# Performance work log

Measured on AMD Instinct MI355X. Metric: run time of the kernel, lower is better.

The kernel has to match this reference:

```python
import jax, jax.numpy as jnp
import numpy as np

USER_NUM = 100000
ITEM_NUM = 50000
N_NODES = USER_NUM + ITEM_NUM
HIDE_DIM = 64
N_EDGES = 4000000
LAYER_NUM = 3


def setup_inputs() -> dict:
    key = jax.random.key(0)
    k1, k2, k3, k4 = jax.random.split(key, 4)
    # Xavier uniform for embeddings: bound = sqrt(6/(fan_in+fan_out))
    bound_u = float(np.sqrt(6.0 / (USER_NUM + HIDE_DIM)))
    bound_i = float(np.sqrt(6.0 / (ITEM_NUM + HIDE_DIM)))
    user_emb = jax.random.uniform(k1, (USER_NUM, HIDE_DIM), jnp.float32, -bound_u, bound_u)
    item_emb = jax.random.uniform(k2, (ITEM_NUM, HIDE_DIM), jnp.float32, -bound_i, bound_i)
    src = jax.random.randint(k3, (N_EDGES,), 0, N_NODES, dtype=jnp.int32)
    dst = jax.random.randint(k4, (N_EDGES,), 0, N_NODES, dtype=jnp.int32)
    return {"user_emb": user_emb, "item_emb": item_emb, "src": src, "dst": dst}


def _gcn_layer(node_f, src, dst, out_norm, in_norm):
    # node_f: [N, D]; symmetric degree-normalized SpMM (copy_u + sum)
    h = node_f * out_norm  # pre-scale by out_degree^-0.5
    agg = jax.ops.segment_sum(h[src], dst, num_segments=N_NODES)
    return agg * in_norm  # post-scale by in_degree^-0.5


def reference(user_emb, item_emb, src, dst):
    ones = jnp.ones((N_EDGES,), jnp.float32)
    out_deg = jnp.clip(jax.ops.segment_sum(ones, src, num_segments=N_NODES), 1.0)
    in_deg = jnp.clip(jax.ops.segment_sum(ones, dst, num_segments=N_NODES), 1.0)
    out_norm = (out_deg ** -0.5)[:, None]
    in_norm = (in_deg ** -0.5)[:, None]

    res_user = user_emb
    res_item = item_emb
    for i in range(LAYER_NUM):
        if i == 0:
            node_f = jnp.concatenate([res_user, res_item], axis=0)
        else:
            node_f = embeddings
        embeddings = _gcn_layer(node_f, src, dst, out_norm, in_norm)
        scale = 1.0 / (i + 2)
        res_user = res_user + embeddings[:USER_NUM] * scale
        res_item = res_item + embeddings[USER_NUM:] * scale
    return (res_user, res_item)
```

## Files before the change

kernel.cpp:

```cpp
#include <hip/hip_runtime.h>
#include <stdint.h>

#define USER_NUM 100000
#define ITEM_NUM 50000
#define N_NODES  150000
#define HIDE_DIM 64
#define N_EDGES  4000000
#define SLAB     72

#define HRANGES 3
#define RNODES  50000
#define RWORDS  (RNODES / 4)
#define SLICES  128
#define EPS     ((N_EDGES + SLICES - 1) / SLICES)

#define BSH     9
#define BNODES  512
#define NBUCK   293
#define SSLICES 640
#define EPSB    (N_EDGES / SSLICES)

__device__ __forceinline__ unsigned short f2bf(float f) {
    union { float f; unsigned int i; } c; c.f = f;
    unsigned int b = c.i;
    return (unsigned short)((b + 0x7FFFu + ((b >> 16) & 1u)) >> 16);
}
__device__ __forceinline__ float lo_bf(uint32_t u) {
    union { uint32_t u; float f; } c; c.u = u << 16; return c.f;
}
__device__ __forceinline__ float hi_bf(uint32_t u) {
    union { uint32_t u; float f; } c; c.u = u & 0xffff0000u; return c.f;
}

__global__ void hist_kernel(const int* __restrict__ src, uint32_t* __restrict__ partial) {
    __shared__ uint32_t bins[RWORDS];
    int r  = blockIdx.x / SLICES;
    int sl = blockIdx.x - r * SLICES;
    for (int i = threadIdx.x; i < RWORDS; i += 512) bins[i] = 0;
    __syncthreads();
    int lo = r * RNODES, hi = lo + RNODES;
    int e0 = sl * EPS;
    int e1 = e0 + EPS; if (e1 > N_EDGES) e1 = N_EDGES;
    for (int e = e0 + threadIdx.x; e < e1; e += 512) {
        int s = src[e];
        if (s >= lo && s < hi) {
            int x = s - lo;
            atomicAdd(&bins[x >> 2], 1u << (8 * (x & 3)));
        }
    }
    __syncthreads();
    uint32_t* out = partial + (size_t)(r * SLICES + sl) * RWORDS;
    for (int i = threadIdx.x; i < RWORDS; i += 512) out[i] = bins[i];
}

__global__ void bhist_kernel(const int* __restrict__ dst, uint32_t* __restrict__ cntA) {
    __shared__ uint32_t cnt[NBUCK];
    int s = blockIdx.x;
    for (int i = threadIdx.x; i < NBUCK; i += 512) cnt[i] = 0;
    __syncthreads();
    int e0 = s * EPSB;
    for (int e = e0 + threadIdx.x; e < e0 + EPSB; e += 512)
        atomicAdd(&cnt[((unsigned)dst[e]) >> BSH], 1u);
    __syncthreads();
    for (int i = threadIdx.x; i < NBUCK; i += 512) cntA[(size_t)s * NBUCK + i] = cnt[i];
}

__global__ void scanA_kernel(const uint32_t* __restrict__ cntA, uint32_t* __restrict__ rel,
                             uint32_t* __restrict__ btot) {
    __shared__ uint32_t sd[SSLICES];
    int b = blockIdx.x;
    int t = threadIdx.x;
    uint32_t v = cntA[(size_t)t * NBUCK + b];
    sd[t] = v;
    __syncthreads();
    for (int off = 1; off < SSLICES; off <<= 1) {
        uint32_t x = (t >= off) ? sd[t - off] : 0;
        __syncthreads();
        sd[t] += x;
        __syncthreads();
    }
    rel[(size_t)t * NBUCK + b] = sd[t] - v;
    if (t == SSLICES - 1) btot[b] = sd[t];
}

__global__ void scanB_kernel(const uint32_t* __restrict__ btot, uint32_t* __restrict__ bbase) {
    __shared__ uint32_t tot[512];
    int t = threadIdx.x;
    uint32_t v = (t < NBUCK) ? btot[t] : 0;
    tot[t] = v;
    __syncthreads();
    for (int off = 1; off < 512; off <<= 1) {
        uint32_t x = (t >= off) ? tot[t - off] : 0;
        __syncthreads();
        tot[t] += x;
        __syncthreads();
    }
    if (t < NBUCK) bbase[t] = tot[t] - v;
    if (t == NBUCK - 1) bbase[NBUCK] = tot[t];
}

__global__ void scatter_kernel(const int* __restrict__ src, const int* __restrict__ dst,
                               const uint32_t* __restrict__ rel, const uint32_t* __restrict__ bbase,
                               uint32_t* __restrict__ sorted) {
    __shared__ uint32_t cnt[NBUCK];
    __shared__ uint32_t excl[NBUCK];
    __shared__ uint32_t gpos0[NBUCK];
    __shared__ uint32_t sarr[512];
    __shared__ uint32_t sval[EPSB];
    __shared__ uint16_t sbkt[EPSB];

    int s = blockIdx.x;
    int t = threadIdx.x;
    for (int i = t; i < NBUCK; i += 512) {
        cnt[i] = 0;
        gpos0[i] = bbase[i] + rel[(size_t)s * NBUCK + i];
    }
    __syncthreads();

    int e0 = s * EPSB;
    for (int e = e0 + t; e < e0 + EPSB; e += 512)
        atomicAdd(&cnt[((unsigned)dst[e]) >> BSH], 1u);
    __syncthreads();

    uint32_t v = (t < NBUCK) ? cnt[t] : 0;
    sarr[t] = v;
    __syncthreads();
    for (int off = 1; off < 512; off <<= 1) {
        uint32_t x = (t >= off) ? sarr[t - off] : 0;
        __syncthreads();
        sarr[t] += x;
        __syncthreads();
    }
    if (t < NBUCK) {
        uint32_t ex = sarr[t] - v;
        excl[t] = ex;
        cnt[t] = ex;
    }
    __syncthreads();

    for (int e = e0 + t; e < e0 + EPSB; e += 512) {
        unsigned d = (unsigned)dst[e];
        int sv = src[e];
        unsigned b = d >> BSH;
        unsigned nib = d & (BNODES - 1);
        uint32_t r = atomicAdd(&cnt[b], 1u);
        sval[r] = (uint32_t)sv | (nib << 18);
        sbkt[r] = (uint16_t)b;
    }
    __syncthreads();

    for (int i = t; i < EPSB; i += 512) {
        unsigned b = sbkt[i];
        sorted[gpos0[b] + ((uint32_t)i - excl[b])] = sval[i];
    }
}

__global__ void slab_kernel(const uint32_t* __restrict__ sorted, const uint32_t* __restrict__ bbase,
                            const uint32_t* __restrict__ partial,
                            int* __restrict__ esrc, int* __restrict__ in_cnt,
                            float* __restrict__ in_norm, float* __restrict__ out_norm) {
    __shared__ uint32_t cur[BNODES];
    int b = blockIdx.x;
    for (int i = threadIdx.x; i < BNODES; i += 512) cur[i] = 0;
    __syncthreads();
    uint32_t start = bbase[b];
    uint32_t n = bbase[b + 1] - start;
    for (uint32_t i = threadIdx.x; i < n; i += 512) {
        uint32_t v = sorted[start + i];
        uint32_t nib = v >> 18;
        uint32_t sc = v & 0x3FFFFu;
        uint32_t r = atomicAdd(&cur[nib], 1u);
        if (r < SLAB) esrc[((size_t)(b << BSH) + nib) * SLAB + r] = (int)sc;
    }
    __syncthreads();
    const unsigned char* p8 = (const unsigned char*)partial;
    for (int nib = threadIdx.x; nib < BNODES; nib += 512) {
        int node = (b << BSH) + nib;
        if (node >= N_NODES) continue;
        int ic = (int)cur[nib];
        in_cnt[node] = ic;
        if (ic < 1) ic = 1;
        in_norm[node] = 1.0f / sqrtf((float)ic);
        int r = node / RNODES;
        int x = node - r * RNODES;
        const unsigned char* base = p8 + (size_t)r * SLICES * RNODES + x;
        int oc = 0;
        for (int s = 0; s < SLICES; ++s) oc += base[(size_t)s * RNODES];
        if (oc < 1) oc = 1;
        out_norm[node] = 1.0f / sqrtf((float)oc);
    }
}

__global__ void init_kernel(const float2* __restrict__ user2, const float2* __restrict__ item2,
                            const float* __restrict__ out_norm, uint32_t* __restrict__ h0) {
    int gid = blockIdx.x * blockDim.x + threadIdx.x;
    if (gid >= N_NODES * 32) return;
    int node = gid >> 5;
    float2 v = (node < USER_NUM) ? user2[gid] : item2[gid - USER_NUM * 32];
    float on = out_norm[node];
    h0[gid] = (uint32_t)f2bf(v.x * on) | ((uint32_t)f2bf(v.y * on) << 16);
}

__global__ void agg_kernel(const uint32_t* __restrict__ h32, const int* __restrict__ esrc,
                           const int* __restrict__ in_cnt,
                           const float* __restrict__ in_norm, const float* __restrict__ out_norm,
                           const float4* __restrict__ user4, const float4* __restrict__ item4,
                           float4* __restrict__ res4, uint4* __restrict__ hn128,
                           float s_prev, float s_cur, int mode) {
    int wid  = (blockIdx.x * blockDim.x + threadIdx.x) >> 6;
    int lane = threadIdx.x & 63;
    int half = lane >> 5;
    int p    = (lane >> 3) & 3;
    int q    = lane & 7;
    int node = wid * 2 + half;
    if (node >= N_NODES) return;

    int deg = in_cnt[node]; if (deg > SLAB) deg = SLAB;
    int beg = node * SLAB;
    int hb  = half << 5;

    int sl0 = lane & 31;
    int idx0 = (sl0      < deg) ? esrc[beg + sl0]      : 0;
    int idx1 = (sl0 + 32 < deg) ? esrc[beg + sl0 + 32] : 0;

    const uint4* h128 = (const uint4*)h32;

    float a0 = 0.f, a1 = 0.f, a2 = 0.f, a3 = 0.f;
    float a4 = 0.f, a5 = 0.f, a6 = 0.f, a7 = 0.f;

#define ACC8(U) do { \
        a0 += lo_bf((U).x); a1 += hi_bf((U).x); \
        a2 += lo_bf((U).y); a3 += hi_bf((U).y); \
        a4 += lo_bf((U).z); a5 += hi_bf((U).z); \
        a6 += lo_bf((U).w); a7 += hi_bf((U).w); } while (0)

    int d0 = (deg < 32) ? deg : 32;
    {
        int sA0 = __shfl(idx0, hb + p,      64);
        int sA1 = __shfl(idx0, hb + 4 + p,  64);
        int sA2 = __shfl(idx0, hb + 8 + p,  64);
        int sA3 = __shfl(idx0, hb + 12 + p, 64);
        uint4 uA0 = h128[sA0 * 8 + q];
        uint4 uA1 = h128[sA1 * 8 + q];
        uint4 uA2 = h128[sA2 * 8 + q];
        uint4 uA3 = h128[sA3 * 8 + q];
        int sB0 = __shfl(idx0, hb + 16 + p, 64);
        int sB1 = __shfl(idx0, hb + 20 + p, 64);
        int sB2 = __shfl(idx0, hb + 24 + p, 64);
        int sB3 = __shfl(idx0, hb + 28 + p, 64);
        uint4 uB0 = h128[sB0 * 8 + q];
        uint4 uB1 = h128[sB1 * 8 + q];
        uint4 uB2 = h128[sB2 * 8 + q];
        uint4 uB3 = h128[sB3 * 8 + q];
        if (p      < d0) ACC8(uA0);
        if (4 + p  < d0) ACC8(uA1);
        if (8 + p  < d0) ACC8(uA2);
        if (12 + p < d0) ACC8(uA3);
        if (16 + p < d0) ACC8(uB0);
        if (20 + p < d0) ACC8(uB1);
        if (24 + p < d0) ACC8(uB2);
        if (28 + p < d0) ACC8(uB3);
    }

    int m1 = ((deg < 64) ? deg : 64) - 32;
    if (m1 > 0) {
        int nj1 = (m1 + 3) >> 2;
        int j = 0;
        for (; 4 * j + 8 <= m1; j += 2) {
            int e0 = 4 * j + p;
            int s0 = __shfl(idx1, hb + e0,     64);
            int s1 = __shfl(idx1, hb + e0 + 4, 64);
            uint4 u0 = h128[s0 * 8 + q];
            uint4 u1 = h128[s1 * 8 + q];
            ACC8(u0);
            ACC8(u1);
        }
        for (; j < nj1; ++j) {
            int e = 4 * j + p;
            int s = __shfl(idx1, hb + e, 64);
            uint4 u = h128[s * 8 + q];
            if (e < m1) ACC8(u);
        }
    }

    for (int e = 64 + p; e < deg; e += 4) {
        int s = esrc[beg + e];
        uint4 u = h128[s * 8 + q];
        ACC8(u);
    }
#undef ACC8

    a0 += __shfl_xor(a0, 8, 64);  a1 += __shfl_xor(a1, 8, 64);
    a2 += __shfl_xor(a2, 8, 64);  a3 += __shfl_xor(a3, 8, 64);
    a4 += __shfl_xor(a4, 8, 64);  a5 += __shfl_xor(a5, 8, 64);
    a6 += __shfl_xor(a6, 8, 64);  a7 += __shfl_xor(a7, 8, 64);
    a0 += __shfl_xor(a0, 16, 64); a1 += __shfl_xor(a1, 16, 64);
    a2 += __shfl_xor(a2, 16, 64); a3 += __shfl_xor(a3, 16, 64);
    a4 += __shfl_xor(a4, 16, 64); a5 += __shfl_xor(a5, 16, 64);
    a6 += __shfl_xor(a6, 16, 64); a7 += __shfl_xor(a7, 16, 64);

    float innorm = in_norm[node];
    float v0 = a0 * innorm, v1 = a1 * innorm, v2 = a2 * innorm, v3 = a3 * innorm;
    float v4 = a4 * innorm, v5 = a5 * innorm, v6 = a6 * innorm, v7 = a7 * innorm;

    if (mode == 0) {
        if (p == 0) {
            float on = out_norm[node];
            uint4 w;
            w.x = (uint32_t)f2bf(v0 * on) | ((uint32_t)f2bf(v1 * on) << 16);
            w.y = (uint32_t)f2bf(v2 * on) | ((uint32_t)f2bf(v3 * on) << 16);
            w.z = (uint32_t)f2bf(v4 * on) | ((uint32_t)f2bf(v5 * on) << 16);
            w.w = (uint32_t)f2bf(v6 * on) | ((uint32_t)f2bf(v7 * on) << 16);
            hn128[node * 8 + q] = w;
        }
    } else if (mode == 1) {
        float on = out_norm[node];
        if (p == 0) {
            uint4 w;
            w.x = (uint32_t)f2bf(v0 * on) | ((uint32_t)f2bf(v1 * on) << 16);
            w.y = (uint32_t)f2bf(v2 * on) | ((uint32_t)f2bf(v3 * on) << 16);
            w.z = (uint32_t)f2bf(v4 * on) | ((uint32_t)f2bf(v5 * on) << 16);
            w.w = (uint32_t)f2bf(v6 * on) | ((uint32_t)f2bf(v7 * on) << 16);
            hn128[node * 8 + q] = w;
        } else if (p <= 2) {
            int of = node * 16 + 2 * q + (p - 1);
            float4 x = (node < USER_NUM) ? user4[of] : item4[of - USER_NUM * 16];
            uint2 hw = ((const uint2*)h32)[of];
            float rinv = 1.0f / on;
            float b0 = (p == 1) ? v0 : v4;
            float b1 = (p == 1) ? v1 : v5;
            float b2 = (p == 1) ? v2 : v6;
            float b3 = (p == 1) ? v3 : v7;
            float4 rv;
            rv.x = x.x + lo_bf(hw.x) * rinv * s_prev + b0 * s_cur;
            rv.y = x.y + hi_bf(hw.x) * rinv * s_prev + b1 * s_cur;
            rv.z = x.z + lo_bf(hw.y) * rinv * s_prev + b2 * s_cur;
            rv.w = x.w + hi_bf(hw.y) * rinv * s_prev + b3 * s_cur;
            res4[of] = rv;
        }
    } else {
        if (p == 1 || p == 2) {
            int of = node * 16 + 2 * q + (p - 1);
            float b0 = (p == 1) ? v0 : v4;
            float b1 = (p == 1) ? v1 : v5;
            float b2 = (p == 1) ? v2 : v6;
            float b3 = (p == 1) ? v3 : v7;
            float4 rv = res4[of];
            rv.x += b0 * s_cur;
            rv.y += b1 * s_cur;
            rv.z += b2 * s_cur;
            rv.w += b3 * s_cur;
            res4[of] = rv;
        }
    }
}

static inline uintptr_t align_up(uintptr_t p, uintptr_t a) { return (p + a - 1) & ~(a - 1); }

extern "C" void kernel_launch(void* const* d_in, const int* in_sizes, int n_in,
                              void* d_out, int out_size, void* d_ws, size_t ws_size,
                              hipStream_t stream) {
    const float* user_emb = (const float*)d_in[0];
    const float* item_emb = (const float*)d_in[1];
    const int*   src      = (const int*)d_in[2];
    const int*   dst      = (const int*)d_in[3];
    float*       res      = (float*)d_out;

    uintptr_t p = (uintptr_t)d_ws;
    int* in_cnt = (int*)p;                     p = align_up(p + (size_t)N_NODES * 4, 128);
    float* out_norm = (float*)p;               p = align_up(p + (size_t)N_NODES * 4, 128);
    float* in_norm = (float*)p;                p = align_up(p + (size_t)N_NODES * 4, 128);
    uint32_t* btot = (uint32_t*)p;             p = align_up(p + (size_t)NBUCK * 4, 128);
    uint32_t* bbase = (uint32_t*)p;            p = align_up(p + (size_t)(NBUCK + 1) * 4, 128);
    int* esrc = (int*)p;                       p = align_up(p + (size_t)NBUCK * BNODES * SLAB * 4, 128);
    uint32_t* hA = (uint32_t*)p;               p = align_up(p + (size_t)N_NODES * 32 * 4, 128);
    uint32_t* hB = (uint32_t*)p;
    uint32_t* sorted  = hA;
    uint32_t* partial = hB;
    uint32_t* cntA    = (uint32_t*)esrc;
    uint32_t* rel     = (uint32_t*)esrc + (size_t)SSLICES * NBUCK;

    const int BT = 256;
    int fb = (N_NODES * 32 + BT - 1) / BT;
    int ab = (N_NODES / 2 * 64 + BT - 1) / BT;

    const float2* user2 = (const float2*)user_emb;
    const float2* item2 = (const float2*)item_emb;
    const float4* user4 = (const float4*)user_emb;
    const float4* item4 = (const float4*)item_emb;

    hist_kernel<<<HRANGES * SLICES, 512, 0, stream>>>(src, partial);
    bhist_kernel<<<SSLICES, 512, 0, stream>>>(dst, cntA);
    scanA_kernel<<<NBUCK, SSLICES, 0, stream>>>(cntA, rel, btot);
    scanB_kernel<<<1, 512, 0, stream>>>(btot, bbase);
    scatter_kernel<<<SSLICES, 512, 0, stream>>>(src, dst, rel, bbase, sorted);
    slab_kernel<<<NBUCK, 512, 0, stream>>>(sorted, bbase, partial, esrc, in_cnt, in_norm, out_norm);
    init_kernel<<<fb, BT, 0, stream>>>(user2, item2, out_norm, hA);

    agg_kernel<<<ab, BT, 0, stream>>>(hA, esrc, in_cnt, in_norm, out_norm, user4, item4,
                                      (float4*)res, (uint4*)hB, 0.0f, 0.0f, 0);
    agg_kernel<<<ab, BT, 0, stream>>>(hB, esrc, in_cnt, in_norm, out_norm, user4, item4,
                                      (float4*)res, (uint4*)hA, 0.5f, 1.0f / 3.0f, 1);
    agg_kernel<<<ab, BT, 0, stream>>>(hA, esrc, in_cnt, in_norm, out_norm, user4, item4,
                                      (float4*)res, (uint4*)hB, 0.0f, 0.25f, 2);
}
```

Before: 430.8 us.

## Fuse preprocessing histograms, use atomic bucket cursors, defer residual write to last layer

New measurement: 427.7 us. About the same (-0.7%).

```diff
diff --git a/kernel.cpp b/kernel.cpp
--- a/kernel.cpp
+++ b/kernel.cpp
@@ -12,7 +12,7 @@
 #define RNODES  50000
 #define RWORDS  (RNODES / 4)
 #define SLICES  128
-#define EPS     ((N_EDGES + SLICES - 1) / SLICES)
+#define EPS     (N_EDGES / SLICES)
 
 #define BSH     9
 #define BNODES  512
@@ -32,58 +32,56 @@
     union { uint32_t u; float f; } c; c.u = u & 0xffff0000u; return c.f;
 }
 
-__global__ void hist_kernel(const int* __restrict__ src, uint32_t* __restrict__ partial) {
+__global__ void histfused_kernel(const int* __restrict__ src, const int* __restrict__ dst,
+                                 uint32_t* __restrict__ partial, uint32_t* __restrict__ btot) {
     __shared__ uint32_t bins[RWORDS];
     int r  = blockIdx.x / SLICES;
     int sl = blockIdx.x - r * SLICES;
-    for (int i = threadIdx.x; i < RWORDS; i += 512) bins[i] = 0;
-    __syncthreads();
-    int lo = r * RNODES, hi = lo + RNODES;
-    int e0 = sl * EPS;
-    int e1 = e0 + EPS; if (e1 > N_EDGES) e1 = N_EDGES;
-    for (int e = e0 + threadIdx.x; e < e1; e += 512) {
-        int s = src[e];
-        if (s >= lo && s < hi) {
-            int x = s - lo;
-            atomicAdd(&bins[x >> 2], 1u << (8 * (x & 3)));
-        }
-    }
-    __syncthreads();
-    uint32_t* out = partial + (size_t)(r * SLICES + sl) * RWORDS;
-    for (int i = threadIdx.x; i < RWORDS; i += 512) out[i] = bins[i];
-}
-
-__global__ void bhist_kernel(const int* __restrict__ dst, uint32_t* __restrict__ cntA) {
-    __shared__ uint32_t cnt[NBUCK];
-    int s = blockIdx.x;
-    for (int i = threadIdx.x; i < NBUCK; i += 512) cnt[i] = 0;
-    __syncthreads();
-    int e0 = s * EPSB;
-    for (int e = e0 + threadIdx.x; e < e0 + EPSB; e += 512)
-        atomicAdd(&cnt[((unsigned)dst[e]) >> BSH], 1u);
-    __syncthreads();
-    for (int i = threadIdx.x; i < NBUCK; i += 512) cntA[(size_t)s * NBUCK + i] = cnt[i];
-}
-
-__global__ void scanA_kernel(const uint32_t* __restrict__ cntA, uint32_t* __restrict__ rel,
-                             uint32_t* __restrict__ btot) {
-    __shared__ uint32_t sd[SSLICES];
-    int b = blockIdx.x;
-    int t = threadIdx.x;
-    uint32_t v = cntA[(size_t)t * NBUCK + b];
-    sd[t] = v;
-    __syncthreads();
-    for (int off = 1; off < SSLICES; off <<= 1) {
-        uint32_t x = (t >= off) ? sd[t - off] : 0;
-        __syncthreads();
-        sd[t] += x;
-        __syncthreads();
-    }
-    rel[(size_t)t * NBUCK + b] = sd[t] - v;
-    if (t == SSLICES - 1) btot[b] = sd[t];
-}
-
-__global__ void scanB_kernel(const uint32_t* __restrict__ btot, uint32_t* __restrict__ bbase) {
+    int e0 = sl * EPS, e1 = e0 + EPS;
+    if (r < HRANGES) {
+        for (int i = threadIdx.x; i < RWORDS; i += 512) bins[i] = 0;
+        __syncthreads();
+        int lo = r * RNODES, hi = lo + RNODES;
+        for (int e = e0 + threadIdx.x; e < e1; e += 512) {
+            int s = src[e];
+            if (s >= lo && s < hi) {
+                int x = s - lo;
+                atomicAdd(&bins[x >> 2], 1u << (8 * (x & 3)));
+            }
+        }
+        __syncthreads();
+        uint32_t* out = partial + (size_t)(r * SLICES + sl) * RWORDS;
+        for (int i = threadIdx.x; i < RWORDS; i += 512) out[i] = bins[i];
+    } else {
+        for (int i = threadIdx.x; i < NBUCK; i += 512) bins[i] = 0;
+        __syncthreads();
+        for (int e = e0 + threadIdx.x; e < e1; e += 512)
+            atomicAdd(&bins[((unsigned)dst[e]) >> BSH], 1u);
+        __syncthreads();
+        for (int i = threadIdx.x; i < NBUCK; i += 512)
+            if (bins[i]) atomicAdd(&btot[i], bins[i]);
+    }
+}
+
+__global__ void rednorm_kernel(const uint32_t* __restrict__ partial, float* __restrict__ out_norm) {
+    int g = blockIdx.x * blockDim.x + threadIdx.x;
+    if (g >= HRANGES * RWORDS) return;
+    int r = g / RWORDS, w = g - r * RWORDS;
+    const uint32_t* p = partial + (size_t)r * SLICES * RWORDS + w;
+    uint32_t acc = 0;
+#pragma unroll 16
+    for (int sl = 0; sl < SLICES; ++sl) acc += p[(size_t)sl * RWORDS];
+    int oc0 = acc & 255, oc1 = (acc >> 8) & 255, oc2 = (acc >> 16) & 255, oc3 = (acc >> 24);
+    float4 o;
+    o.x = 1.0f / sqrtf((float)(oc0 < 1 ? 1 : oc0));
+    o.y = 1.0f / sqrtf((float)(oc1 < 1 ? 1 : oc1));
+    o.z = 1.0f / sqrtf((float)(oc2 < 1 ? 1 : oc2));
+    o.w = 1.0f / sqrtf((float)(oc3 < 1 ? 1 : oc3));
+    ((float4*)out_norm)[(size_t)r * (RNODES / 4) + w] = o;
+}
+
+__global__ void scanB_kernel(const uint32_t* __restrict__ btot, uint32_t* __restrict__ bbase,
+                             uint32_t* __restrict__ gcur) {
     __shared__ uint32_t tot[512];
     int t = threadIdx.x;
     uint32_t v = (t < NBUCK) ? btot[t] : 0;
@@ -95,13 +93,12 @@
         tot[t] += x;
         __syncthreads();
     }
-    if (t < NBUCK) bbase[t] = tot[t] - v;
+    if (t < NBUCK) { uint32_t ex = tot[t] - v; bbase[t] = ex; gcur[t] = ex; }
     if (t == NBUCK - 1) bbase[NBUCK] = tot[t];
 }
 
 __global__ void scatter_kernel(const int* __restrict__ src, const int* __restrict__ dst,
-                               const uint32_t* __restrict__ rel, const uint32_t* __restrict__ bbase,
-                               uint32_t* __restrict__ sorted) {
+                               uint32_t* __restrict__ gcur, uint32_t* __restrict__ sorted) {
     __shared__ uint32_t cnt[NBUCK];
     __shared__ uint32_t excl[NBUCK];
     __shared__ uint32_t gpos0[NBUCK];
@@ -111,10 +108,7 @@
 
     int s = blockIdx.x;
     int t = threadIdx.x;
-    for (int i = t; i < NBUCK; i += 512) {
-        cnt[i] = 0;
-        gpos0[i] = bbase[i] + rel[(size_t)s * NBUCK + i];
-    }
+    for (int i = t; i < NBUCK; i += 512) cnt[i] = 0;
     __syncthreads();
 
     int e0 = s * EPSB;
@@ -122,8 +116,8 @@
         atomicAdd(&cnt[((unsigned)dst[e]) >> BSH], 1u);
     __syncthreads();
 
-    uint32_t v = (t < NBUCK) ? cnt[t] : 0;
-    sarr[t] = v;
+    uint32_t myc = (t < NBUCK) ? cnt[t] : 0;
+    sarr[t] = myc;
     __syncthreads();
     for (int off = 1; off < 512; off <<= 1) {
         uint32_t x = (t >= off) ? sarr[t - off] : 0;
@@ -132,9 +126,10 @@
         __syncthreads();
     }
     if (t < NBUCK) {
-        uint32_t ex = sarr[t] - v;
+        uint32_t ex = sarr[t] - myc;
         excl[t] = ex;
         cnt[t] = ex;
+        if (myc) gpos0[t] = atomicAdd(&gcur[t], myc);
     }
     __syncthreads();
 
@@ -156,9 +151,8 @@
 }
 
 __global__ void slab_kernel(const uint32_t* __restrict__ sorted, const uint32_t* __restrict__ bbase,
-                            const uint32_t* __restrict__ partial,
                             int* __restrict__ esrc, int* __restrict__ in_cnt,
-                            float* __restrict__ in_norm, float* __restrict__ out_norm) {
+                            float* __restrict__ in_norm) {
     __shared__ uint32_t cur[BNODES];
     int b = blockIdx.x;
     for (int i = threadIdx.x; i < BNODES; i += 512) cur[i] = 0;
@@ -173,7 +167,6 @@
         if (r < SLAB) esrc[((size_t)(b << BSH) + nib) * SLAB + r] = (int)sc;
     }
     __syncthreads();
-    const unsigned char* p8 = (const unsigned char*)partial;
     for (int nib = threadIdx.x; nib < BNODES; nib += 512) {
         int node = (b << BSH) + nib;
         if (node >= N_NODES) continue;
@@ -181,13 +174,6 @@
         in_cnt[node] = ic;
         if (ic < 1) ic = 1;
         in_norm[node] = 1.0f / sqrtf((float)ic);
-        int r = node / RNODES;
-        int x = node - r * RNODES;
-        const unsigned char* base = p8 + (size_t)r * SLICES * RNODES + x;
-        int oc = 0;
-        for (int s = 0; s < SLICES; ++s) oc += base[(size_t)s * RNODES];
-        if (oc < 1) oc = 1;
-        out_norm[node] = 1.0f / sqrtf((float)oc);
     }
 }
 
@@ -206,7 +192,8 @@
                            const float* __restrict__ in_norm, const float* __restrict__ out_norm,
                            const float4* __restrict__ user4, const float4* __restrict__ item4,
                            float4* __restrict__ res4, uint4* __restrict__ hn128,
-                           float s_prev, float s_cur, int mode) {
+                           const uint2* __restrict__ h1own,
+                           float s1, float s2, float s3, int mode) {
     int wid  = (blockIdx.x * blockDim.x + threadIdx.x) >> 6;
     int lane = threadIdx.x & 63;
     int half = lane >> 5;
@@ -269,9 +256,9 @@
         for (; 4 * j + 8 <= m1; j += 2) {
             int e0 = 4 * j + p;
             int s0 = __shfl(idx1, hb + e0,     64);
-            int s1 = __shfl(idx1, hb + e0 + 4, 64);
+            int s1g = __shfl(idx1, hb + e0 + 4, 64);
             uint4 u0 = h128[s0 * 8 + q];
-            uint4 u1 = h128[s1 * 8 + q];
+            uint4 u1 = h128[s1g * 8 + q];
             ACC8(u0);
             ACC8(u1);
         }
@@ -313,43 +300,22 @@
             w.w = (uint32_t)f2bf(v6 * on) | ((uint32_t)f2bf(v7 * on) << 16);
             hn128[node * 8 + q] = w;
         }
-    } else if (mode == 1) {
-        float on = out_norm[node];
-        if (p == 0) {
-            uint4 w;
-            w.x = (uint32_t)f2bf(v0 * on) | ((uint32_t)f2bf(v1 * on) << 16);
-            w.y = (uint32_t)f2bf(v2 * on) | ((uint32_t)f2bf(v3 * on) << 16);
-            w.z = (uint32_t)f2bf(v4 * on) | ((uint32_t)f2bf(v5 * on) << 16);
-            w.w = (uint32_t)f2bf(v6 * on) | ((uint32_t)f2bf(v7 * on) << 16);
-            hn128[node * 8 + q] = w;
-        } else if (p <= 2) {
+    } else {
+        if (p == 1 || p == 2) {
             int of = node * 16 + 2 * q + (p - 1);
             float4 x = (node < USER_NUM) ? user4[of] : item4[of - USER_NUM * 16];
-            uint2 hw = ((const uint2*)h32)[of];
-            float rinv = 1.0f / on;
+            uint2 h1 = h1own[of];
+            uint2 h2 = ((const uint2*)h32)[of];
+            float rinv = 1.0f / out_norm[node];
             float b0 = (p == 1) ? v0 : v4;
             float b1 = (p == 1) ? v1 : v5;
             float b2 = (p == 1) ? v2 : v6;
             float b3 = (p == 1) ? v3 : v7;
             float4 rv;
-            rv.x = x.x + lo_bf(hw.x) * rinv * s_prev + b0 * s_cur;
-            rv.y = x.y + hi_bf(hw.x) * rinv * s_prev + b1 * s_cur;
-            rv.z = x.z + lo_bf(hw.y) * rinv * s_prev + b2 * s_cur;
-            rv.w = x.w + hi_bf(hw.y) * rinv * s_prev + b3 * s_cur;
-            res4[of] = rv;
-        }
-    } else {
-        if (p == 1 || p == 2) {
-            int of = node * 16 + 2 * q + (p - 1);
-            float b0 = (p == 1) ? v0 : v4;
-            float b1 = (p == 1) ? v1 : v5;
-            float b2 = (p == 1) ? v2 : v6;
-            float b3 = (p == 1) ? v3 : v7;
-            float4 rv = res4[of];
-            rv.x += b0 * s_cur;
-            rv.y += b1 * s_cur;
-            rv.z += b2 * s_cur;
-            rv.w += b3 * s_cur;
+            rv.x = x.x + (lo_bf(h1.x) * s1 + lo_bf(h2.x) * s2) * rinv + b0 * s3;
+            rv.y = x.y + (hi_bf(h1.x) * s1 + hi_bf(h2.x) * s2) * rinv + b1 * s3;
+            rv.z = x.z + (lo_bf(h1.y) * s1 + lo_bf(h2.y) * s2) * rinv + b2 * s3;
+            rv.w = x.w + (hi_bf(h1.y) * s1 + hi_bf(h2.y) * s2) * rinv + b3 * s3;
             res4[of] = rv;
         }
     }
@@ -372,13 +338,12 @@
     float* in_norm = (float*)p;                p = align_up(p + (size_t)N_NODES * 4, 128);
     uint32_t* btot = (uint32_t*)p;             p = align_up(p + (size_t)NBUCK * 4, 128);
     uint32_t* bbase = (uint32_t*)p;            p = align_up(p + (size_t)(NBUCK + 1) * 4, 128);
+    uint32_t* gcur = (uint32_t*)p;             p = align_up(p + (size_t)NBUCK * 4, 128);
     int* esrc = (int*)p;                       p = align_up(p + (size_t)NBUCK * BNODES * SLAB * 4, 128);
     uint32_t* hA = (uint32_t*)p;               p = align_up(p + (size_t)N_NODES * 32 * 4, 128);
     uint32_t* hB = (uint32_t*)p;
     uint32_t* sorted  = hA;
     uint32_t* partial = hB;
-    uint32_t* cntA    = (uint32_t*)esrc;
-    uint32_t* rel     = (uint32_t*)esrc + (size_t)SSLICES * NBUCK;
 
     const int BT = 256;
     int fb = (N_NODES * 32 + BT - 1) / BT;
@@ -389,18 +354,21 @@
     const float4* user4 = (const float4*)user_emb;
     const float4* item4 = (const float4*)item_emb;
 
-    hist_kernel<<<HRANGES * SLICES, 512, 0, stream>>>(src, partial);
-    bhist_kernel<<<SSLICES, 512, 0, stream>>>(dst, cntA);
-    scanA_kernel<<<NBUCK, SSLICES, 0, stream>>>(cntA, rel, btot);
-    scanB_kernel<<<1, 512, 0, stream>>>(btot, bbase);
-    scatter_kernel<<<SSLICES, 512, 0, stream>>>(src, dst, rel, bbase, sorted);
-    slab_kernel<<<NBUCK, 512, 0, stream>>>(sorted, bbase, partial, esrc, in_cnt, in_norm, out_norm);
+    hipMemsetAsync(btot, 0, (size_t)NBUCK * 4, stream);
+    histfused_kernel<<<(HRANGES + 1) * SLICES, 512, 0, stream>>>(src, dst, partial, btot);
+    rednorm_kernel<<<(HRANGES * RWORDS + 255) / 256, 256, 0, stream>>>(partial, out_norm);
+    scanB_kernel<<<1, 512, 0, stream>>>(btot, bbase, gcur);
+    scatter_kernel<<<SSLICES, 512, 0, stream>>>(src, dst, gcur, sorted);
+    slab_kernel<<<NBUCK, 512, 0, stream>>>(sorted, bbase, esrc, in_cnt, in_norm);
     init_kernel<<<fb, BT, 0, stream>>>(user2, item2, out_norm, hA);
 
     agg_kernel<<<ab, BT, 0, stream>>>(hA, esrc, in_cnt, in_norm, out_norm, user4, item4,
-                                      (float4*)res, (uint4*)hB, 0.0f, 0.0f, 0);
+                                      (float4*)res, (uint4*)hB, (const uint2*)hB,
+                                      0.0f, 0.0f, 0.0f, 0);
     agg_kernel<<<ab, BT, 0, stream>>>(hB, esrc, in_cnt, in_norm, out_norm, user4, item4,
-                                      (float4*)res, (uint4*)hA, 0.5f, 1.0f / 3.0f, 1);
+                                      (float4*)res, (uint4*)hA, (const uint2*)hB,
+                                      0.0f, 0.0f, 0.0f, 0);
     agg_kernel<<<ab, BT, 0, stream>>>(hA, esrc, in_cnt, in_norm, out_norm, user4, item4,
-                                      (float4*)res, (uint4*)hB, 0.0f, 0.25f, 2);
-}
+                                      (float4*)res, (uint4*)hB, (const uint2*)hB,
+                                      0.5f, 1.0f / 3.0f, 0.25f, 1);
+}
```
